# Kernel optimization log

Hardware: AMD Instinct MI355X
Metric: run time of the kernel (lower is better)

The kernel has to match this reference:

```python
import jax, jax.numpy as jnp
import numpy as np

D_MODEL = 256
D_STATE = 128          # d_model // 2
D_CONV = 4
EXPAND = 4
D_INNER = EXPAND * D_MODEL  # 1024
DT_RANK = (D_MODEL + 15) // 16  # 16
N_HEADS = 8
D_FF = 4 * D_MODEL
EPS = 1e-6


def layer_norm(x, a, b):
    # torch LayerNorm-like but with unbiased std (ddof=1) per the source
    mean = jnp.mean(x, axis=-1, keepdims=True)
    d = x.shape[-1]
    var = jnp.sum((x - mean) ** 2, axis=-1, keepdims=True) / (d - 1)
    std = jnp.sqrt(var)
    return a * (x - mean) / (std + EPS) + b


def silu(x):
    return x * jax.nn.sigmoid(x)


def mamba(x, in_proj_w, conv_w, conv_b, x_proj_w, dt_proj_w, dt_proj_b, A_log, Dp, out_proj_w):
    B, L, _ = x.shape
    xz = jnp.einsum('bld,ed->ble', x, in_proj_w)  # (B,L,2*D_INNER)
    xi, z = xz[..., :D_INNER], xz[..., D_INNER:]
    # causal depthwise conv1d over L
    xp = jnp.pad(xi, ((0, 0), (D_CONV - 1, 0), (0, 0)))
    u = conv_b
    for k in range(D_CONV):
        u = u + xp[:, k:k + L, :] * conv_w[:, k]
    u = silu(u)  # (B,L,D_INNER)
    dbl = jnp.einsum('bld,ed->ble', u, x_proj_w)  # (B,L,DT_RANK+2*D_STATE)
    dt = dbl[..., :DT_RANK]
    Bm = dbl[..., DT_RANK:DT_RANK + D_STATE]
    Cm = dbl[..., DT_RANK + D_STATE:]
    dt = jax.nn.softplus(jnp.einsum('blr,dr->bld', dt, dt_proj_w) + dt_proj_b)  # (B,L,D_INNER)
    A = -jnp.exp(A_log)  # (D_INNER, D_STATE)
    dA = jnp.exp(jnp.einsum('bld,dn->bldn', dt, A))          # (B,L,Din,N)
    dBu = jnp.einsum('bld,bln,bld->bldn', dt, Bm, u)          # (B,L,Din,N)

    def step(h, inp):
        dA_t, dBu_t, C_t = inp
        h = dA_t * h + dBu_t                    # (B,Din,N)
        y = jnp.einsum('bdn,bn->bd', h, C_t)    # (B,Din)
        return h, y

    h0 = jnp.zeros((B, D_INNER, D_STATE), dtype=x.dtype)
    _, ys = jax.lax.scan(step, h0, (jnp.swapaxes(dA, 0, 1), jnp.swapaxes(dBu, 0, 1), jnp.swapaxes(Cm, 0, 1)))
    y = jnp.swapaxes(ys, 0, 1) + u * Dp  # (B,L,Din)
    y = y * silu(z)
    return jnp.einsum('ble,de->bld', y, out_proj_w)


def cross_attention(q_in, kv_in, mask, wq_w, wq_b, wk_w, wk_b, wv_w, wv_b, wo_w, wo_b):
    B, Lq, _ = q_in.shape
    Lk = kv_in.shape[1]
    dk = D_MODEL // N_HEADS
    q = (jnp.einsum('bld,ed->ble', q_in, wq_w) + wq_b).reshape(B, Lq, N_HEADS, dk).transpose(0, 2, 1, 3)
    k = (jnp.einsum('bld,ed->ble', kv_in, wk_w) + wk_b).reshape(B, Lk, N_HEADS, dk).transpose(0, 2, 1, 3)
    v = (jnp.einsum('bld,ed->ble', kv_in, wv_w) + wv_b).reshape(B, Lk, N_HEADS, dk).transpose(0, 2, 1, 3)
    scores = jnp.einsum('bhqd,bhkd->bhqk', q, k) / np.sqrt(dk)
    # mask: (B,1,Lk) bool -> broadcast (B,1,1,Lk)
    scores = jnp.where(mask[:, None, :, :], scores, jnp.finfo(scores.dtype).min)
    p = jax.nn.softmax(scores, axis=-1)
    o = jnp.einsum('bhqk,bhkd->bhqd', p, v).transpose(0, 2, 1, 3).reshape(B, Lq, D_MODEL)
    return jnp.einsum('ble,de->bld', o, wo_w) + wo_b


def setup_inputs() -> dict:
    key = jax.random.key(0)
    ks = jax.random.split(key, 24)
    s = 0.02
    B, L, Lm = 2, 512, 512
    inp = {
        'x': jax.random.normal(ks[0], (B, L, D_MODEL), jnp.float32),
        'memory': jax.random.normal(ks[1], (B, Lm, D_MODEL), jnp.float32),
        'src_mask': jnp.ones((B, 1, Lm), bool),
        'tgt_mask': jnp.ones((B, 1, L), bool),
        # mamba params
        'in_proj_w': jax.random.normal(ks[2], (2 * D_INNER, D_MODEL)) * s,
        'conv_w': jax.random.normal(ks[3], (D_INNER, D_CONV)) * s,
        'conv_b': jnp.zeros((D_INNER,)),
        'x_proj_w': jax.random.normal(ks[4], (DT_RANK + 2 * D_STATE, D_INNER)) * s,
        'dt_proj_w': jax.random.normal(ks[5], (D_INNER, DT_RANK)) * s,
        'dt_proj_b': jnp.log(jnp.expm1(0.01)) * jnp.ones((D_INNER,)),
        'A_log': jnp.log(jnp.broadcast_to(jnp.arange(1, D_STATE + 1, dtype=jnp.float32), (D_INNER, D_STATE))),
        'Dp': jnp.ones((D_INNER,)),
        'out_proj_w': jax.random.normal(ks[6], (D_MODEL, D_INNER)) * s,
        # norms
        'norm1_a': jnp.ones((D_MODEL,)), 'norm1_b': jnp.zeros((D_MODEL,)),
        'norm2_a': jnp.ones((D_MODEL,)), 'norm2_b': jnp.zeros((D_MODEL,)),
        'norm3_a': jnp.ones((D_MODEL,)), 'norm3_b': jnp.zeros((D_MODEL,)),
        # cross attention
        'wq_w': jax.random.normal(ks[7], (D_MODEL, D_MODEL)) * s, 'wq_b': jnp.zeros((D_MODEL,)),
        'wk_w': jax.random.normal(ks[8], (D_MODEL, D_MODEL)) * s, 'wk_b': jnp.zeros((D_MODEL,)),
        'wv_w': jax.random.normal(ks[9], (D_MODEL, D_MODEL)) * s, 'wv_b': jnp.zeros((D_MODEL,)),
        'wo_w': jax.random.normal(ks[10], (D_MODEL, D_MODEL)) * s, 'wo_b': jnp.zeros((D_MODEL,)),
        # ffn
        'w1_w': jax.random.normal(ks[11], (D_FF, D_MODEL)) * s, 'w1_b': jnp.zeros((D_FF,)),
        'w2_w': jax.random.normal(ks[12], (D_MODEL, D_FF)) * s, 'w2_b': jnp.zeros((D_MODEL,)),
    }
    return inp


def reference(x, memory, src_mask, tgt_mask,
              in_proj_w, conv_w, conv_b, x_proj_w, dt_proj_w, dt_proj_b, A_log, Dp, out_proj_w,
              norm1_a, norm1_b, norm2_a, norm2_b, norm3_a, norm3_b,
              wq_w, wq_b, wk_w, wk_b, wv_w, wv_b, wo_w, wo_b,
              w1_w, w1_b, w2_w, w2_b):
    # self mamba block (pre-norm, residual); dropout = 0
    h = x + mamba(layer_norm(x, norm1_a, norm1_b), in_proj_w, conv_w, conv_b,
                  x_proj_w, dt_proj_w, dt_proj_b, A_log, Dp, out_proj_w)
    # cross attention block
    h = h + cross_attention(layer_norm(h, norm2_a, norm2_b), memory, src_mask,
                            wq_w, wq_b, wk_w, wk_b, wv_w, wv_b, wo_w, wo_b)
    # ffn block
    hn = layer_norm(h, norm3_a, norm3_b)
    ff = jnp.einsum('blf,df->bld', jax.nn.relu(jnp.einsum('bld,fd->blf', hn, w1_w) + w1_b), w2_w) + w2_b
    return h + ff
```

## Files before the change

### kernel.cpp

```cpp
#include <hip/hip_runtime.h>
#include <hip/hip_bf16.h>

#define B_SZ 2
#define L_SEQ 512
#define D_MODEL 256
#define D_STATE 128
#define D_CONV 4
#define D_INNER 1024
#define DT_RANK 16
#define N_HEADS 8
#define DK 32
#define D_FF 1024
#define R_TOT (B_SZ * L_SEQ)
#define DBL_LD (DT_RANK + 2 * D_STATE)
#define NSEG 16
#define SEGL 32

typedef __hip_bfloat16 bf16;
typedef __attribute__((ext_vector_type(8))) short short8;
typedef __attribute__((ext_vector_type(4))) float floatx4;

__device__ inline float fexp(float x) { return __expf(x); }
__device__ inline float frcp(float x) { return __builtin_amdgcn_rcpf(x); }
__device__ inline float silu_f(float x) { return x * frcp(1.f + fexp(-x)); }
__device__ inline float softplus_f(float x) { return (x > 20.f) ? x : __logf(1.f + fexp(x)); }
__device__ inline float bf2f(unsigned short u) { return __uint_as_float(((unsigned)u) << 16); }

__device__ inline float dpp_sum64(float x) {
    x += __int_as_float(__builtin_amdgcn_update_dpp(0, __float_as_int(x), 0x111, 0xf, 0xf, true));
    x += __int_as_float(__builtin_amdgcn_update_dpp(0, __float_as_int(x), 0x112, 0xf, 0xf, true));
    x += __int_as_float(__builtin_amdgcn_update_dpp(0, __float_as_int(x), 0x114, 0xf, 0xf, true));
    x += __int_as_float(__builtin_amdgcn_update_dpp(0, __float_as_int(x), 0x118, 0xf, 0xf, true));
    x += __int_as_float(__builtin_amdgcn_update_dpp(0, __float_as_int(x), 0x142, 0xf, 0xf, true));
    x += __int_as_float(__builtin_amdgcn_update_dpp(0, __float_as_int(x), 0x143, 0xf, 0xf, true));
    return x;
}

#define S_MEM 262144
#define S_INW 524288
#define S_XPW 278528
#define S_OPW 262144
#define S_WQ  65536
#define S_WK  65536
#define S_WV  65536
#define S_WO  65536
#define S_W1  262144
#define S_W2  262144
#define S_TOT (S_MEM+S_INW+S_XPW+S_OPW+S_WQ+S_WK+S_WV+S_WO+S_W1+S_W2)
#define PACK_BLKS ((S_TOT + 255) / 256)
#define Z1_F4 (4 * R_TOT * D_MODEL / 4)
#define Z2_F4 (R_TOT * D_MODEL / 4)
#define Z3_F4 (R_TOT * DBL_LD / 4)
#define ZERO_BLKS ((Z1_F4 + Z2_F4 + Z3_F4 + 255) / 256)

__global__ __launch_bounds__(256) void pack_ln1(
    const float* __restrict__ s0, const float* __restrict__ s1,
    const float* __restrict__ s2, const float* __restrict__ s3,
    const float* __restrict__ s4, const float* __restrict__ s5,
    const float* __restrict__ s6, const float* __restrict__ s7,
    const float* __restrict__ s8, const float* __restrict__ s9,
    bf16* __restrict__ dst,
    const float* __restrict__ X, const float* __restrict__ a,
    const float* __restrict__ bvec, bf16* __restrict__ ln1b,
    float* __restrict__ zero1, float* __restrict__ zero2,
    float* __restrict__ zero3)
{
    __shared__ float r1[256], r2[256];
    if (blockIdx.x < PACK_BLKS) {
        const long i = (long)blockIdx.x * 256 + threadIdx.x;
        if (i >= S_TOT) return;
        const long off[11] = {0, S_MEM, S_MEM+S_INW, S_MEM+S_INW+S_XPW,
            S_MEM+S_INW+S_XPW+S_OPW, S_MEM+S_INW+S_XPW+S_OPW+S_WQ,
            S_MEM+S_INW+S_XPW+S_OPW+S_WQ+S_WK,
            S_MEM+S_INW+S_XPW+S_OPW+S_WQ+S_WK+S_WV,
            S_MEM+S_INW+S_XPW+S_OPW+S_WQ+S_WK+S_WV+S_WO,
            S_MEM+S_INW+S_XPW+S_OPW+S_WQ+S_WK+S_WV+S_WO+S_W1, S_TOT};
        const float* srcs[10] = {s0,s1,s2,s3,s4,s5,s6,s7,s8,s9};
        int seg = 0;
#pragma unroll
        for (int k = 1; k < 10; ++k) if (i >= off[k]) seg = k;
        dst[i] = __float2bfloat16(srcs[seg][i - off[seg]]);
    } else if (blockIdx.x < PACK_BLKS + R_TOT) {
        const int row = blockIdx.x - PACK_BLKS;
        const int t = threadIdx.x;
        const float v = X[(long)row * D_MODEL + t];
        r1[t] = v;
        r2[t] = v * v;
        __syncthreads();
        for (int s = 128; s > 0; s >>= 1) {
            if (t < s) { r1[t] += r1[t + s]; r2[t] += r2[t + s]; }
            __syncthreads();
        }
        const float mean = r1[0] * (1.f / 256.f);
        const float var = (r2[0] - 256.f * mean * mean) * (1.f / 255.f);
        const float sd = sqrtf(fmaxf(var, 0.f));
        const float o = a[t] * (v - mean) / (sd + 1e-6f) + bvec[t];
        ln1b[(long)row * D_MODEL + t] = __float2bfloat16(o);
    } else {
        const long i4 = (long)(blockIdx.x - PACK_BLKS - R_TOT) * 256 + threadIdx.x;
        const float4 z = {0.f, 0.f, 0.f, 0.f};
        if (i4 < Z1_F4)                      *(float4*)&zero1[i4 * 4] = z;
        else if (i4 < Z1_F4 + Z2_F4)          *(float4*)&zero2[(i4 - Z1_F4) * 4] = z;
        else if (i4 < Z1_F4 + Z2_F4 + Z3_F4)  *(float4*)&zero3[(i4 - Z1_F4 - Z2_F4) * 4] = z;
    }
}

template <int EPI>
__global__ __launch_bounds__(256) void mfma_gemm(
    const bf16* __restrict__ A, const bf16* __restrict__ W, int K,
    float* __restrict__ C, bf16* __restrict__ Cb, int ldc,
    const float* __restrict__ bias, const float* __restrict__ res,
    int M, int N)
{
    const int wave = threadIdx.x >> 6;
    const int lane = threadIdx.x & 63;
    const int row16 = lane & 15;
    const int quad  = lane >> 4;
    const int bm = blockIdx.y * 64 + wave * 16;
    const int bn = blockIdx.x * 64;

    floatx4 acc[4];
#pragma unroll
    for (int t = 0; t < 4; ++t) acc[t] = (floatx4){0.f, 0.f, 0.f, 0.f};

    const long arow = (long)(bm + row16) * K;
    for (int k0 = 0; k0 < K; k0 += 32) {
        const short8 av = *(const short8*)(A + arow + k0 + quad * 8);
#pragma unroll
        for (int t = 0; t < 4; ++t) {
            const int gn = bn + t * 16 + row16;
            short8 bv = {0,0,0,0,0,0,0,0};
            if (gn < N) bv = *(const short8*)(W + (long)gn * K + k0 + quad * 8);
            acc[t] = __builtin_amdgcn_mfma_f32_16x16x32_bf16(av, bv, acc[t], 0, 0, 0);
        }
    }

#pragma unroll
    for (int t = 0; t < 4; ++t) {
        const int gn = bn + t * 16 + row16;
        if (gn >= N) continue;
        const float bs = bias ? bias[gn] : 0.f;
#pragma unroll
        for (int r = 0; r < 4; ++r) {
            const int gm = bm + quad * 4 + r;
            float v = acc[t][r] + bs;
            if (EPI == 1) v = fmaxf(v, 0.f);
            const long ci = (long)gm * ldc + gn;
            if (res) v += res[ci];
            if (C)  C[ci] = v;
            if (Cb) Cb[ci] = __float2bfloat16(v);
        }
    }
}

template <int SK>
__global__ __launch_bounds__(256) void splitk_gemm(
    const bf16* __restrict__ A, const bf16* __restrict__ W, int K,
    float* __restrict__ C, int ldc,
    const float* __restrict__ bias, const float* __restrict__ res,
    int M, int N)
{
    const int wave = threadIdx.x >> 6;
    const int lane = threadIdx.x & 63;
    const int row16 = lane & 15;
    const int quad  = lane >> 4;
    const int bm = blockIdx.y * 64 + wave * 16;
    const int bn = blockIdx.x * 64;
    const int kz = blockIdx.z;
    const int ksl = K / SK;
    const int kbeg = kz * ksl;

    floatx4 acc[4];
#pragma unroll
    for (int t = 0; t < 4; ++t) acc[t] = (floatx4){0.f, 0.f, 0.f, 0.f};

    const long arow = (long)(bm + row16) * K;
    for (int k0 = kbeg; k0 < kbeg + ksl; k0 += 32) {
        const short8 av = *(const short8*)(A + arow + k0 + quad * 8);
#pragma unroll
        for (int t = 0; t < 4; ++t) {
            const int gn = bn + t * 16 + row16;
            short8 bv = {0,0,0,0,0,0,0,0};
            if (gn < N) bv = *(const short8*)(W + (long)gn * K + k0 + quad * 8);
            acc[t] = __builtin_amdgcn_mfma_f32_16x16x32_bf16(av, bv, acc[t], 0, 0, 0);
        }
    }

#pragma unroll
    for (int t = 0; t < 4; ++t) {
        const int gn = bn + t * 16 + row16;
        if (gn >= N) continue;
        const float bs = (kz == 0 && bias) ? bias[gn] : 0.f;
#pragma unroll
        for (int r = 0; r < 4; ++r) {
            const int gm = bm + quad * 4 + r;
            float v = acc[t][r] + bs;
            const long ci = (long)gm * ldc + gn;
            if (kz == 0 && res) v += res[ci];
            atomicAdd(&C[ci], v);
        }
    }
}

__global__ __launch_bounds__(256) void xproj_kv_gemm(
    const bf16* __restrict__ ub, const bf16* __restrict__ XPWb,
    float* __restrict__ dbl,
    const bf16* __restrict__ memb, const bf16* __restrict__ WKb,
    const bf16* __restrict__ WVb,
    const float* __restrict__ WKB, const float* __restrict__ WVB,
    float* __restrict__ kb, float* __restrict__ vb)
{
    const int wave = threadIdx.x >> 6;
    const int lane = threadIdx.x & 63;
    const int row16 = lane & 15;
    const int quad  = lane >> 4;
    const int bm = blockIdx.y * 64 + wave * 16;
    const int bn = blockIdx.x * 64;
    const int z = blockIdx.z;

    const bf16* A; const bf16* W; const float* bias; float* C;
    int K, N, ldc, kbeg, ksl;
    if (z < 4) {
        A = ub; W = XPWb; bias = nullptr; C = dbl;
        K = D_INNER; N = DBL_LD; ldc = DBL_LD;
        ksl = D_INNER / 4; kbeg = z * ksl;
    } else {
        if (bn >= D_MODEL) return;
        const int zz = z - 4;
        const int which = zz >> 1;
        const int kz = zz & 1;
        A = memb; W = which ? WVb : WKb;
        bias = (kz == 0) ? (which ? WVB : WKB) : nullptr;
        C = which ? vb : kb;
        K = D_MODEL; N = D_MODEL; ldc = D_MODEL;
        ksl = D_MODEL / 2; kbeg = kz * ksl;
    }

    floatx4 acc[4];
#pragma unroll
    for (int t = 0; t < 4; ++t) acc[t] = (floatx4){0.f, 0.f, 0.f, 0.f};

    const long arow = (long)(bm + row16) * K;
    for (int k0 = kbeg; k0 < kbeg + ksl; k0 += 32) {
        const short8 av = *(const short8*)(A + arow + k0 + quad * 8);
#pragma unroll
        for (int t = 0; t < 4; ++t) {
            const int gn = bn + t * 16 + row16;
            short8 bv = {0,0,0,0,0,0,0,0};
            if (gn < N) bv = *(const short8*)(W + (long)gn * K + k0 + quad * 8);
            acc[t] = __builtin_amdgcn_mfma_f32_16x16x32_bf16(av, bv, acc[t], 0, 0, 0);
        }
    }

#pragma unroll
    for (int t = 0; t < 4; ++t) {
        const int gn = bn + t * 16 + row16;
        if (gn >= N) continue;
        const float bs = bias ? bias[gn] : 0.f;
#pragma unroll
        for (int r = 0; r < 4; ++r) {
            const int gm = bm + quad * 4 + r;
            atomicAdd(&C[(long)gm * ldc + gn], acc[t][r] + bs);
        }
    }
}

__global__ __launch_bounds__(256) void q_gemm(
    const bf16* __restrict__ ln2b, const bf16* __restrict__ WQb,
    const float* __restrict__ WQB, float* __restrict__ qb)
{
    const int wave = threadIdx.x >> 6;
    const int lane = threadIdx.x & 63;
    const int row16 = lane & 15;
    const int quad  = lane >> 4;
    const int bm = blockIdx.y * 64 + wave * 16;
    const int bn = blockIdx.x * 64;
    const int kz = blockIdx.z;
    const int kbeg = kz * (D_MODEL / 2);

    floatx4 acc[4];
#pragma unroll
    for (int t = 0; t < 4; ++t) acc[t] = (floatx4){0.f, 0.f, 0.f, 0.f};

    const long arow = (long)(bm + row16) * D_MODEL;
    for (int k0 = kbeg; k0 < kbeg + D_MODEL / 2; k0 += 32) {
        const short8 av = *(const short8*)(ln2b + arow + k0 + quad * 8);
#pragma unroll
        for (int t = 0; t < 4; ++t) {
            const int gn = bn + t * 16 + row16;
            const short8 bv = *(const short8*)(WQb + (long)gn * D_MODEL + k0 + quad * 8);
            acc[t] = __builtin_amdgcn_mfma_f32_16x16x32_bf16(av, bv, acc[t], 0, 0, 0);
        }
    }
#pragma unroll
    for (int t = 0; t < 4; ++t) {
        const int gn = bn + t * 16 + row16;
        const float bs = (kz == 0) ? WQB[gn] : 0.f;
#pragma unroll
        for (int r = 0; r < 4; ++r) {
            const int gm = bm + quad * 4 + r;
            atomicAdd(&qb[(long)gm * D_MODEL + gn], acc[t][r] + bs);
        }
    }
}

__global__ __launch_bounds__(256) void gemm16_ln(
    const bf16* __restrict__ A, const bf16* __restrict__ W, int K,
    const float* __restrict__ bias, const float* __restrict__ res,
    float* __restrict__ Cf,
    const float* __restrict__ lna, const float* __restrict__ lnb,
    bf16* __restrict__ lnout)
{
    __shared__ float tile[16][264];
    __shared__ float red1[16][16];
    __shared__ float red2[16][16];
    const int w = threadIdx.x >> 6;
    const int lane = threadIdx.x & 63;
    const int row16 = lane & 15;
    const int quad  = lane >> 4;
    const int bm = blockIdx.x * 16;

    floatx4 acc[4];
#pragma unroll
    for (int t = 0; t < 4; ++t) acc[t] = (floatx4){0.f, 0.f, 0.f, 0.f};

    const long arow = (long)(bm + row16) * K;
    for (int k0 = 0; k0 < K; k0 += 32) {
        const short8 av = *(const short8*)(A + arow + k0 + quad * 8);
#pragma unroll
        for (int t = 0; t < 4; ++t) {
            const int gn = w * 64 + t * 16 + row16;
            const short8 bv = *(const short8*)(W + (long)gn * K + k0 + quad * 8);
            acc[t] = __builtin_amdgcn_mfma_f32_16x16x32_bf16(av, bv, acc[t], 0, 0, 0);
        }
    }

#pragma unroll
    for (int t = 0; t < 4; ++t) {
        const int gn = w * 64 + t * 16 + row16;
        const float bs = bias ? bias[gn] : 0.f;
#pragma unroll
        for (int r = 0; r < 4; ++r) {
            const int gm = bm + quad * 4 + r;
            float v = acc[t][r] + bs;
            const long ci = (long)gm * D_MODEL + gn;
            if (res) v += res[ci];
            Cf[ci] = v;
            tile[quad * 4 + r][gn] = v;
        }
    }
    __syncthreads();

    const int r = threadIdx.x >> 4;
    const int g = threadIdx.x & 15;
    float s = 0.f, q = 0.f;
#pragma unroll
    for (int i = 0; i < 16; ++i) {
        const float x = tile[r][g * 16 + i];
        s += x; q += x * x;
    }
    red1[r][g] = s; red2[r][g] = q;
    __syncthreads();
    float ts = 0.f, tq = 0.f;
#pragma unroll
    for (int i = 0; i < 16; ++i) { ts += red1[r][i]; tq += red2[r][i]; }
    const float mean = ts * (1.f / 256.f);
    const float var = (tq - 256.f * mean * mean) * (1.f / 255.f);
    const float sd = sqrtf(fmaxf(var, 0.f));
    const long rowbase = (long)(bm + r) * D_MODEL;
#pragma unroll
    for (int i = 0; i < 16; ++i) {
        const int c = g * 16 + i;
        const float o = lna[c] * (tile[r][c] - mean) / (sd + 1e-6f) + lnb[c];
        lnout[rowbase + c] = __float2bfloat16(o);
    }
}

__global__ __launch_bounds__(256) void ln_kernel(
    const float* __restrict__ x, const float* __restrict__ a,
    const float* __restrict__ bvec, bf16* __restrict__ out)
{
    const int row = blockIdx.x;
    const int t = threadIdx.x;
    const float v = x[(long)row * D_MODEL + t];
    __shared__ float r1[256], r2[256];
    r1[t] = v;
    r2[t] = v * v;
    __syncthreads();
    for (int s = 128; s > 0; s >>= 1) {
        if (t < s) { r1[t] += r1[t + s]; r2[t] += r2[t + s]; }
        __syncthreads();
    }
    const float mean = r1[0] * (1.f / 256.f);
    const float var = (r2[0] - 256.f * mean * mean) * (1.f / 255.f);
    const float sd = sqrtf(fmaxf(var, 0.f));
    const float o = a[t] * (v - mean) / (sd + 1e-6f) + bvec[t];
    out[(long)row * D_MODEL + t] = __float2bfloat16(o);
}

__global__ __launch_bounds__(256) void dt_gemm_T(
    const float* __restrict__ A , const float* __restrict__ W ,
    const float* __restrict__ bias, float* __restrict__ dtT)
{
    __shared__ float As[DT_RANK][65];
    __shared__ float Bs[DT_RANK][65];
    __shared__ float Ct[64][65];
    const int bm = blockIdx.y * 64;
    const int bn = blockIdx.x * 64;
    const int tid = threadIdx.x;
    const int tx = tid & 15;
    const int ty = tid >> 4;
    const int r = tid >> 2;
    const int kk = (tid & 3) * 4;
#pragma unroll
    for (int q = 0; q < 4; ++q) {
        As[kk + q][r] = A[(long)(bm + r) * DBL_LD + kk + q];
        Bs[kk + q][r] = W[(long)(bn + r) * DT_RANK + kk + q];
    }
    __syncthreads();
    float acc[4][4] = {};
#pragma unroll
    for (int k = 0; k < DT_RANK; ++k) {
        float a[4], bv[4];
#pragma unroll
        for (int i = 0; i < 4; ++i) a[i] = As[k][ty * 4 + i];
#pragma unroll
        for (int j = 0; j < 4; ++j) bv[j] = Bs[k][tx * 4 + j];
#pragma unroll
        for (int i = 0; i < 4; ++i)
#pragma unroll
            for (int j = 0; j < 4; ++j)
                acc[i][j] = fmaf(a[i], bv[j], acc[i][j]);
    }
#pragma unroll
    for (int i = 0; i < 4; ++i)
#pragma unroll
        for (int j = 0; j < 4; ++j)
            Ct[tx * 4 + j][ty * 4 + i] = softplus_f(acc[i][j] + bias[bn + tx * 4 + j]);
    __syncthreads();
    const int b = bm >> 9;
    const int l0 = bm & 511;
    const int r2 = tid >> 4;
    const int c4 = (tid & 15) * 4;
#pragma unroll
    for (int q = 0; q < 4; ++q) {
        const int dl = r2 + q * 16;
        float4 v = {Ct[dl][c4], Ct[dl][c4 + 1], Ct[dl][c4 + 2], Ct[dl][c4 + 3]};
        *(float4*)&dtT[((long)(b * D_INNER + bn + dl) << 9) + l0 + c4] = v;
    }
}

__global__ __launch_bounds__(256) void conv_silu_T(
    const bf16* __restrict__ xz, const float* __restrict__ cw,
    const float* __restrict__ cb, bf16* __restrict__ ub, float* __restrict__ uT)
{
    __shared__ float t[64][65];
    const int db = blockIdx.x;
    const int lb = blockIdx.y;
    const int b  = blockIdx.z;
    const int tid = threadIdx.x;
    const int r  = tid >> 4;
    const int c4 = (tid & 15) * 4;
    const int d0 = db * 64 + c4;

    const float4 cb4 = *(const float4*)&cb[d0];
    float cwa[4][4];
#pragma unroll
    for (int i = 0; i < 4; ++i) {
        const float4 w = *(const float4*)&cw[(d0 + i) * 4];
        cwa[i][0] = w.x; cwa[i][1] = w.y; cwa[i][2] = w.z; cwa[i][3] = w.w;
    }

#pragma unroll
    for (int q = 0; q < 4; ++q) {
        const int ll = r + q * 16;
        const int l = lb * 64 + ll;
        float s0 = cb4.x, s1 = cb4.y, s2 = cb4.z, s3 = cb4.w;
#pragma unroll
        for (int k = 0; k < D_CONV; ++k) {
            const int ls = l - 3 + k;
            if (ls >= 0) {
                const ushort4 xv = *(const ushort4*)&xz[((long)(b * L_SEQ + ls)) * (2 * D_INNER) + d0];
                s0 = fmaf(bf2f(xv.x), cwa[0][k], s0);
                s1 = fmaf(bf2f(xv.y), cwa[1][k], s1);
                s2 = fmaf(bf2f(xv.z), cwa[2][k], s2);
                s3 = fmaf(bf2f(xv.w), cwa[3][k], s3);
            }
        }
        s0 = silu_f(s0); s1 = silu_f(s1); s2 = silu_f(s2); s3 = silu_f(s3);
        bf16 b0 = __float2bfloat16(s0), b1 = __float2bfloat16(s1);
        bf16 b2 = __float2bfloat16(s2), b3 = __float2bfloat16(s3);
        ushort4 pk;
        pk.x = *reinterpret_cast<unsigned short*>(&b0);
        pk.y = *reinterpret_cast<unsigned short*>(&b1);
        pk.z = *reinterpret_cast<unsigned short*>(&b2);
        pk.w = *reinterpret_cast<unsigned short*>(&b3);
        *reinterpret_cast<ushort4*>(ub + ((long)(b * L_SEQ + l)) * D_INNER + d0) = pk;
        t[c4 + 0][ll] = s0; t[c4 + 1][ll] = s1;
        t[c4 + 2][ll] = s2; t[c4 + 3][ll] = s3;
    }
    __syncthreads();
#pragma unroll
    for (int q = 0; q < 4; ++q) {
        const int dl = r + q * 16;
        float4 v = {t[dl][c4], t[dl][c4 + 1], t[dl][c4 + 2], t[dl][c4 + 3]};
        *(float4*)&uT[((long)(b * D_INNER + db * 64 + dl) << 9) + lb * 64 + c4] = v;
    }
}

__global__ __launch_bounds__(1024) void scan_fused(
    const float* __restrict__ dtT, const float* __restrict__ uT,
    const float* __restrict__ dbl, const float* __restrict__ A_log,
    float* __restrict__ ysT)
{
    const int cd = blockIdx.x;
    const int b = cd >> 10;
    const int d = cd & 1023;
    const int w = threadIdx.x >> 6;
    const int lane = threadIdx.x & 63;
    const int n0 = lane * 2;

    __shared__ float Sh[NSEG][D_STATE];
    __shared__ float Ph[NSEG][D_STATE];

    const float An0 = -fexp(A_log[(long)d * D_STATE + n0]);
    const float An1 = -fexp(A_log[(long)d * D_STATE + n0 + 1]);

    const float* dtp = dtT + ((long)cd << 9) + w * SEGL;
    const float* up  = uT  + ((long)cd << 9) + w * SEGL;
    const float* blp = dbl + ((long)(b * L_SEQ + w * SEGL)) * DBL_LD + DT_RANK + n0;
    const float* clp = blp + D_STATE;

    if (w < NSEG - 1) {
        float h0 = 0.f, h1 = 0.f, sdt = 0.f;
        for (int s = 0; s < SEGL / 8; ++s) {
            const float4 dt0 = *(const float4*)(dtp + s * 8);
            const float4 dt1 = *(const float4*)(dtp + s * 8 + 4);
            const float4 u0  = *(const float4*)(up + s * 8);
            const float4 u1  = *(const float4*)(up + s * 8 + 4);
            float2 Bv[8];
#pragma unroll
            for (int j = 0; j < 8; ++j)
                Bv[j] = *(const float2*)(blp + (long)(s * 8 + j) * DBL_LD);
            const float dts[8] = {dt0.x, dt0.y, dt0.z, dt0.w, dt1.x, dt1.y, dt1.z, dt1.w};
            const float us[8]  = {u0.x,  u0.y,  u0.z,  u0.w,  u1.x,  u1.y,  u1.z,  u1.w};
#pragma unroll
            for (int j = 0; j < 8; ++j) {
                const float dtv = dts[j];
                sdt += dtv;
                const float dtu = dtv * us[j];
                h0 = fmaf(fexp(dtv * An0), h0, dtu * Bv[j].x);
                h1 = fmaf(fexp(dtv * An1), h1, dtu * Bv[j].y);
            }
        }
        Sh[w][n0] = h0; Sh[w][n0 + 1] = h1;
        Ph[w][n0] = fexp(An0 * sdt); Ph[w][n0 + 1] = fexp(An1 * sdt);
    }
    __syncthreads();

    float h0 = 0.f, h1 = 0.f;
    for (int s = 0; s < w; ++s) {
        h0 = fmaf(Ph[s][n0],     h0, Sh[s][n0]);
        h1 = fmaf(Ph[s][n0 + 1], h1, Sh[s][n0 + 1]);
    }

    float* ysp = ysT + ((long)cd << 9) + w * SEGL;
    for (int s = 0; s < SEGL / 8; ++s) {
        const float4 dt0 = *(const float4*)(dtp + s * 8);
        const float4 dt1 = *(const float4*)(dtp + s * 8 + 4);
        const float4 u0  = *(const float4*)(up + s * 8);
        const float4 u1  = *(const float4*)(up + s * 8 + 4);
        float2 Bv[8], Cv[8];
#pragma unroll
        for (int j = 0; j < 8; ++j) {
            Bv[j] = *(const float2*)(blp + (long)(s * 8 + j) * DBL_LD);
            Cv[j] = *(const float2*)(clp + (long)(s * 8 + j) * DBL_LD);
        }
        const float dts[8] = {dt0.x, dt0.y, dt0.z, dt0.w, dt1.x, dt1.y, dt1.z, dt1.w};
        const float us[8]  = {u0.x,  u0.y,  u0.z,  u0.w,  u1.x,  u1.y,  u1.z,  u1.w};
        float yp[8];
#pragma unroll
        for (int j = 0; j < 8; ++j) {
            const float dtv = dts[j];
            const float dtu = dtv * us[j];
            h0 = fmaf(fexp(dtv * An0), h0, dtu * Bv[j].x);
            h1 = fmaf(fexp(dtv * An1), h1, dtu * Bv[j].y);
            yp[j] = fmaf(h0, Cv[j].x, h1 * Cv[j].y);
        }
#pragma unroll
        for (int j = 0; j < 8; ++j) yp[j] = dpp_sum64(yp[j]);

        if (lane == 63) {
            *(float4*)(ysp + s * 8)     = (float4){yp[0], yp[1], yp[2], yp[3]};
            *(float4*)(ysp + s * 8 + 4) = (float4){yp[4], yp[5], yp[6], yp[7]};
        }
    }
}

__global__ __launch_bounds__(256) void gate_kernel(
    const float* __restrict__ ysT, const float* __restrict__ uT,
    const float* __restrict__ Dp, const bf16* __restrict__ xz,
    bf16* __restrict__ y)
{
    __shared__ float t[64][65];
    __shared__ float t2[64][65];
    const int db = blockIdx.x;
    const int lb = blockIdx.y;
    const int b  = blockIdx.z;
    const int tid = threadIdx.x;
    const int r  = tid >> 4;
    const int c4 = (tid & 15) * 4;

#pragma unroll
    for (int q = 0; q < 4; ++q) {
        const int dr = r + q * 16;
        const long base = (((long)(b * D_INNER + db * 64 + dr)) << 9) + lb * 64 + c4;
        const float4 v = *(const float4*)&ysT[base];
        const float4 w = *(const float4*)&uT[base];
        t[dr][c4 + 0] = v.x; t[dr][c4 + 1] = v.y;
        t[dr][c4 + 2] = v.z; t[dr][c4 + 3] = v.w;
        t2[dr][c4 + 0] = w.x; t2[dr][c4 + 1] = w.y;
        t2[dr][c4 + 2] = w.z; t2[dr][c4 + 3] = w.w;
    }
    __syncthreads();

    const float4 dp4 = *(const float4*)&Dp[db * 64 + c4];
#pragma unroll
    for (int q = 0; q < 4; ++q) {
        const int lr = r + q * 16;
        const long row = (long)b * L_SEQ + lb * 64 + lr;
        const ushort4 zu = *(const ushort4*)&xz[row * 2 * D_INNER + D_INNER + db * 64 + c4];
        const float r0 = (t[c4 + 0][lr] + t2[c4 + 0][lr] * dp4.x) * silu_f(bf2f(zu.x));
        const float r1 = (t[c4 + 1][lr] + t2[c4 + 1][lr] * dp4.y) * silu_f(bf2f(zu.y));
        const float r2 = (t[c4 + 2][lr] + t2[c4 + 2][lr] * dp4.z) * silu_f(bf2f(zu.z));
        const float r3 = (t[c4 + 3][lr] + t2[c4 + 3][lr] * dp4.w) * silu_f(bf2f(zu.w));
        bf16 b0 = __float2bfloat16(r0), b1 = __float2bfloat16(r1);
        bf16 b2 = __float2bfloat16(r2), b3 = __float2bfloat16(r3);
        ushort4 pk;
        pk.x = *reinterpret_cast<unsigned short*>(&b0);
        pk.y = *reinterpret_cast<unsigned short*>(&b1);
        pk.z = *reinterpret_cast<unsigned short*>(&b2);
        pk.w = *reinterpret_cast<unsigned short*>(&b3);
        *reinterpret_cast<ushort4*>(y + row * D_INNER + db * 64 + c4) = pk;
    }
}

#define QT 16
#define CK 64

__global__ __launch_bounds__(256) void attn_kernel(
    const float* __restrict__ q, const float* __restrict__ k,
    const float* __restrict__ v, bf16* __restrict__ o)
{
    const int qt = blockIdx.x;
    const int hh = blockIdx.y;
    const int b  = blockIdx.z;
    const int t = threadIdx.x;
    const int lane = t & 15;
    const int qa = t >> 4;
    const int q0 = qt * QT + qa;

    __shared__ float Ks[CK][36];
    __shared__ float Vs[CK][36];

    const float scale = 0.17677669529663687f;
    float qr0[32];
    {
        const float* q0p = q + ((long)(b * L_SEQ + q0) * D_MODEL + hh * DK);
#pragma unroll
        for (int i = 0; i < 8; ++i) {
            const float4 a = *(const float4*)&q0p[i * 4];
            qr0[i*4+0] = a.x * scale; qr0[i*4+1] = a.y * scale;
            qr0[i*4+2] = a.z * scale; qr0[i*4+3] = a.w * scale;
        }
    }

    float m0 = -1e30f, l0 = 0.f, o0[32] = {};

    for (int c = 0; c < L_SEQ; c += CK) {
        __syncthreads();
        {
            const int fid = t * 2;
            const int row = fid >> 3;
            const int c0  = (fid & 7) * 4;
            const float* kp = k + ((long)(b * L_SEQ + c + row) * D_MODEL + hh * DK + c0);
            const float* vp = v + ((long)(b * L_SEQ + c + row) * D_MODEL + hh * DK + c0);
            *(float4*)&Ks[row][c0]     = *(const float4*)kp;
            *(float4*)&Ks[row][c0 + 4] = *(const float4*)(kp + 4);
            *(float4*)&Vs[row][c0]     = *(const float4*)vp;
            *(float4*)&Vs[row][c0 + 4] = *(const float4*)(vp + 4);
        }
        __syncthreads();

        float s0[4];
#pragma unroll
        for (int i = 0; i < 4; ++i) {
            const int kk = i * 16 + lane;
            float a0 = 0.f;
#pragma unroll
            for (int dd = 0; dd < 32; dd += 4) {
                const float4 kv = *(const float4*)&Ks[kk][dd];
                a0 = fmaf(qr0[dd+0], kv.x, a0); a0 = fmaf(qr0[dd+1], kv.y, a0);
                a0 = fmaf(qr0[dd+2], kv.z, a0); a0 = fmaf(qr0[dd+3], kv.w, a0);
            }
            s0[i] = a0;
        }

        float cm0 = s0[0];
#pragma unroll
        for (int i = 1; i < 4; ++i) cm0 = fmaxf(cm0, s0[i]);
#pragma unroll
        for (int off = 8; off > 0; off >>= 1)
            cm0 = fmaxf(cm0, __shfl_down(cm0, off, 16));
        cm0 = __shfl(cm0, 0, 16);

        const float nm0 = fmaxf(m0, cm0);
        const float al0 = fexp(m0 - nm0);
        l0 *= al0;
#pragma unroll
        for (int dd = 0; dd < 32; ++dd) o0[dd] *= al0;
        m0 = nm0;

        float p0[4];
#pragma unroll
        for (int i = 0; i < 4; ++i) { p0[i] = fexp(s0[i] - m0); l0 += p0[i]; }

#pragma unroll
        for (int i = 0; i < 4; ++i) {
            const int kk = i * 16 + lane;
#pragma unroll
            for (int dd = 0; dd < 32; dd += 4) {
                const float4 vv = *(const float4*)&Vs[kk][dd];
                o0[dd+0] = fmaf(p0[i], vv.x, o0[dd+0]);
                o0[dd+1] = fmaf(p0[i], vv.y, o0[dd+1]);
                o0[dd+2] = fmaf(p0[i], vv.z, o0[dd+2]);
                o0[dd+3] = fmaf(p0[i], vv.w, o0[dd+3]);
            }
        }
    }

#pragma unroll
    for (int off = 8; off > 0; off >>= 1) {
        l0 += __shfl_down(l0, off, 16);
#pragma unroll
        for (int dd = 0; dd < 32; ++dd) o0[dd] += __shfl_down(o0[dd], off, 16);
    }
    if (lane == 0) {
        const float i0 = 1.f / l0;
        bf16* op0 = o + ((long)(b * L_SEQ + q0) * D_MODEL + hh * DK);
#pragma unroll
        for (int dd = 0; dd < 32; ++dd) op0[dd] = __float2bfloat16(o0[dd] * i0);
    }
}


extern "C" void kernel_launch(void* const* d_in, const int* in_sizes, int n_in,
                              void* d_out, int out_size, void* d_ws, size_t ws_size,
                              hipStream_t stream) {
    const float* X   = (const float*)d_in[0];
    const float* MEM = (const float*)d_in[1];
    const float* CW  = (const float*)d_in[5];
    const float* CB  = (const float*)d_in[6];
    const float* DTW = (const float*)d_in[8];
    const float* DTB = (const float*)d_in[9];
    const float* ALG = (const float*)d_in[10];
    const float* DP  = (const float*)d_in[11];
    const float* N1A = (const float*)d_in[13];
    const float* N1B = (const float*)d_in[14];
    const float* N2A = (const float*)d_in[15];
    const float* N2B = (const float*)d_in[16];
    const float* N3A = (const float*)d_in[17];
    const float* N3B = (const float*)d_in[18];
    const float* WQB = (const float*)d_in[20];
    const float* WKB = (const float*)d_in[22];
    const float* WVB = (const float*)d_in[24];
    const float* WOB = (const float*)d_in[26];
    const float* W1B = (const float*)d_in[28];
    const float* W2B = (const float*)d_in[30];
    const float* INW = (const float*)d_in[4];
    const float* XPW = (const float*)d_in[7];
    const float* OPW = (const float*)d_in[12];
    const float* WQ  = (const float*)d_in[19];
    const float* WKw = (const float*)d_in[21];
    const float* WVw = (const float*)d_in[23];
    const float* WO  = (const float*)d_in[25];
    const float* W1  = (const float*)d_in[27];
    const float* W2  = (const float*)d_in[29];
    float* out = (float*)d_out;

    bf16* bp = (bf16*)d_ws;
    bf16* ub   = bp;  bp += (long)R_TOT * D_INNER;
    bf16* ybb  = bp;  bp += (long)R_TOT * D_INNER;
    bf16* ffab = ybb;
    bf16* xzb  = bp;  bp += (long)R_TOT * 2 * D_INNER;
    bf16* ln1b = bp;  bp += (long)R_TOT * D_MODEL;
    bf16* aob  = ln1b;
    bf16* ln2b = bp;  bp += (long)R_TOT * D_MODEL;
    bf16* ln3b = ln2b;
    bf16* arena = bp; bp += S_TOT;
    bf16* MEMb = arena;
    bf16* INWb = MEMb + S_MEM;
    bf16* XPWb = INWb + S_INW;
    bf16* OPWb = XPWb + S_XPW;
    bf16* WQb  = OPWb + S_OPW;
    bf16* WKb  = WQb + S_WQ;
    bf16* WVb  = WKb + S_WK;
    bf16* WOb  = WVb + S_WV;
    bf16* W1b  = WOb + S_WO;
    bf16* W2b  = W1b + S_W1;

    float* p = (float*)(bp + ((((long)(bp - (bf16*)d_ws)) & 1) ? 1 : 0));
    float* uT  = p;                                  p += (long)R_TOT * D_INNER;
    float* dbl = p;                                  p += (long)R_TOT * DBL_LD;
    float* dtT = p;                                  p += (long)R_TOT * D_INNER;
    float* ysT = p;                                  p += (long)R_TOT * D_INNER;
    float* h1  = p;                                  p += (long)R_TOT * D_MODEL;
    float* qb  = p;                                  p += (long)R_TOT * D_MODEL;
    float* kb  = p;                                  p += (long)R_TOT * D_MODEL;
    float* vb  = p;                                  p += (long)R_TOT * D_MODEL;
    float* h2  = p;                                  p += (long)R_TOT * D_MODEL;

    const dim3 blk256(256);
    const int MT64 = R_TOT / 64;

    pack_ln1<<<PACK_BLKS + R_TOT + ZERO_BLKS, blk256, 0, stream>>>(
        MEM, INW, XPW, OPW, WQ, WKw, WVw, WO, W1, W2, arena,
        X, N1A, N1B, ln1b, h1, out, dbl);

    mfma_gemm<0><<<dim3(2 * D_INNER / 64, MT64), blk256, 0, stream>>>(
        ln1b, INWb, D_MODEL, nullptr, xzb, 2 * D_INNER, nullptr, nullptr,
        R_TOT, 2 * D_INNER);

    conv_silu_T<<<dim3(D_INNER / 64, L_SEQ / 64, B_SZ), blk256, 0, stream>>>(
        xzb, CW, CB, ub, uT);

    xproj_kv_gemm<<<dim3((DBL_LD + 63) / 64, MT64, 8), blk256, 0, stream>>>(
        ub, XPWb, dbl, MEMb, WKb, WVb, WKB, WVB, kb, vb);

    dt_gemm_T<<<dim3(D_INNER / 64, MT64), blk256, 0, stream>>>(dbl, DTW, DTB, dtT);

    scan_fused<<<B_SZ * D_INNER, dim3(1024), 0, stream>>>(dtT, uT, dbl, ALG, ysT);

    gate_kernel<<<dim3(D_INNER / 64, L_SEQ / 64, B_SZ), blk256, 0, stream>>>(
        ysT, uT, DP, xzb, ybb);

    splitk_gemm<4><<<dim3(D_MODEL / 64, MT64, 4), blk256, 0, stream>>>(
        ybb, OPWb, D_INNER, h1, D_MODEL, nullptr, X, R_TOT, D_MODEL);

    ln_kernel<<<R_TOT, blk256, 0, stream>>>(h1, N2A, N2B, ln2b);

    q_gemm<<<dim3(D_MODEL / 64, MT64, 2), blk256, 0, stream>>>(ln2b, WQb, WQB, qb);

    attn_kernel<<<dim3(L_SEQ / QT, N_HEADS, B_SZ), blk256, 0, stream>>>(qb, kb, vb, aob);

    gemm16_ln<<<R_TOT / 16, blk256, 0, stream>>>(
        aob, WOb, D_MODEL, WOB, h1, h2, N3A, N3B, ln3b);

    mfma_gemm<1><<<dim3(D_FF / 64, MT64), blk256, 0, stream>>>(
        ln3b, W1b, D_MODEL, nullptr, ffab, D_FF, W1B, nullptr, R_TOT, D_FF);

    splitk_gemm<4><<<dim3(D_MODEL / 64, MT64, 4), blk256, 0, stream>>>(
        ffab, W2b, D_FF, out, D_MODEL, W2B, h2, R_TOT, D_MODEL);

    (void)in_sizes; (void)n_in; (void)out_size; (void)ws_size;
}
```

Baseline: 376.2 us.

## Process four channels per scan block and use transpose-reduce for outputs

The selective scan kernel now handles four D_INNER channels per block, so each B/C row load from dbl is reused across four channels and fewer blocks are launched. The per-timestep 64-lane reduction is replaced by a butterfly transpose-reduce (bpermute, ds_swizzle, dpp) that reduces eight outputs at once. Exponentials switch to exp2 with A pre-scaled by log2(e). The cost is more registers per thread and lower occupancy at 1024 threads per block, plus scattered scalar stores for ys.

```diff
diff --git a/kernel.cpp b/kernel.cpp
--- a/kernel.cpp
+++ b/kernel.cpp
@@ -15,12 +15,14 @@
 #define DBL_LD (DT_RANK + 2 * D_STATE)
 #define NSEG 16
 #define SEGL 32
+#define DPB 4
 
 typedef __hip_bfloat16 bf16;
 typedef __attribute__((ext_vector_type(8))) short short8;
 typedef __attribute__((ext_vector_type(4))) float floatx4;
 
 __device__ inline float fexp(float x) { return __expf(x); }
+__device__ inline float fexp2(float x) { return __builtin_amdgcn_exp2f(x); }
 __device__ inline float frcp(float x) { return __builtin_amdgcn_rcpf(x); }
 __device__ inline float silu_f(float x) { return x * frcp(1.f + fexp(-x)); }
 __device__ inline float softplus_f(float x) { return (x > 20.f) ? x : __logf(1.f + fexp(x)); }
@@ -34,6 +36,13 @@
     x += __int_as_float(__builtin_amdgcn_update_dpp(0, __float_as_int(x), 0x142, 0xf, 0xf, true));
     x += __int_as_float(__builtin_amdgcn_update_dpp(0, __float_as_int(x), 0x143, 0xf, 0xf, true));
     return x;
+}
+
+__device__ inline float swz_xor16(float x) {
+    return __int_as_float(__builtin_amdgcn_ds_swizzle(__float_as_int(x), 0x401F));
+}
+__device__ inline float swz_xor8(float x) {
+    return __int_as_float(__builtin_amdgcn_ds_swizzle(__float_as_int(x), 0x201F));
 }
 
 #define S_MEM 262144
@@ -513,86 +522,130 @@
     const float* __restrict__ dbl, const float* __restrict__ A_log,
     float* __restrict__ ysT)
 {
-    const int cd = blockIdx.x;
-    const int b = cd >> 10;
-    const int d = cd & 1023;
+    const int b  = blockIdx.x >> 8;
+    const int d0 = (blockIdx.x & 255) * DPB;
     const int w = threadIdx.x >> 6;
     const int lane = threadIdx.x & 63;
     const int n0 = lane * 2;
 
-    __shared__ float Sh[NSEG][D_STATE];
-    __shared__ float Ph[NSEG][D_STATE];
-
-    const float An0 = -fexp(A_log[(long)d * D_STATE + n0]);
-    const float An1 = -fexp(A_log[(long)d * D_STATE + n0 + 1]);
-
-    const float* dtp = dtT + ((long)cd << 9) + w * SEGL;
-    const float* up  = uT  + ((long)cd << 9) + w * SEGL;
+    __shared__ float Sh[NSEG][DPB][D_STATE];
+    __shared__ float Ph[NSEG][DPB][D_STATE];
+
+    float An0[DPB], An1[DPB];
+#pragma unroll
+    for (int di = 0; di < DPB; ++di) {
+        An0[di] = -fexp(A_log[(long)(d0 + di) * D_STATE + n0]) * 1.44269504f;
+        An1[di] = -fexp(A_log[(long)(d0 + di) * D_STATE + n0 + 1]) * 1.44269504f;
+    }
+
     const float* blp = dbl + ((long)(b * L_SEQ + w * SEGL)) * DBL_LD + DT_RANK + n0;
     const float* clp = blp + D_STATE;
+    const long tbase = ((long)(b * D_INNER + d0) << 9) + w * SEGL;
 
     if (w < NSEG - 1) {
-        float h0 = 0.f, h1 = 0.f, sdt = 0.f;
+        float h0[DPB] = {}, h1[DPB] = {}, sdt[DPB] = {};
         for (int s = 0; s < SEGL / 8; ++s) {
-            const float4 dt0 = *(const float4*)(dtp + s * 8);
-            const float4 dt1 = *(const float4*)(dtp + s * 8 + 4);
-            const float4 u0  = *(const float4*)(up + s * 8);
-            const float4 u1  = *(const float4*)(up + s * 8 + 4);
             float2 Bv[8];
 #pragma unroll
             for (int j = 0; j < 8; ++j)
                 Bv[j] = *(const float2*)(blp + (long)(s * 8 + j) * DBL_LD);
-            const float dts[8] = {dt0.x, dt0.y, dt0.z, dt0.w, dt1.x, dt1.y, dt1.z, dt1.w};
-            const float us[8]  = {u0.x,  u0.y,  u0.z,  u0.w,  u1.x,  u1.y,  u1.z,  u1.w};
-#pragma unroll
-            for (int j = 0; j < 8; ++j) {
-                const float dtv = dts[j];
-                sdt += dtv;
-                const float dtu = dtv * us[j];
-                h0 = fmaf(fexp(dtv * An0), h0, dtu * Bv[j].x);
-                h1 = fmaf(fexp(dtv * An1), h1, dtu * Bv[j].y);
+#pragma unroll
+            for (int di = 0; di < DPB; ++di) {
+                const float* dtp = dtT + tbase + ((long)di << 9) + s * 8;
+                const float* up  = uT  + tbase + ((long)di << 9) + s * 8;
+                const float4 dt0 = *(const float4*)dtp;
+                const float4 dt1 = *(const float4*)(dtp + 4);
+                const float4 u0  = *(const float4*)up;
+                const float4 u1  = *(const float4*)(up + 4);
+                const float dts[8] = {dt0.x, dt0.y, dt0.z, dt0.w, dt1.x, dt1.y, dt1.z, dt1.w};
+                const float us[8]  = {u0.x,  u0.y,  u0.z,  u0.w,  u1.x,  u1.y,  u1.z,  u1.w};
+#pragma unroll
+                for (int j = 0; j < 8; ++j) {
+                    const float dtv = dts[j];
+                    sdt[di] += dtv;
+                    const float dtu = dtv * us[j];
+                    h0[di] = fmaf(fexp2(dtv * An0[di]), h0[di], dtu * Bv[j].x);
+                    h1[di] = fmaf(fexp2(dtv * An1[di]), h1[di], dtu * Bv[j].y);
+                }
             }
         }
-        Sh[w][n0] = h0; Sh[w][n0 + 1] = h1;
-        Ph[w][n0] = fexp(An0 * sdt); Ph[w][n0 + 1] = fexp(An1 * sdt);
+#pragma unroll
+        for (int di = 0; di < DPB; ++di) {
+            Sh[w][di][n0]     = h0[di];
+            Sh[w][di][n0 + 1] = h1[di];
+            Ph[w][di][n0]     = fexp2(An0[di] * sdt[di]);
+            Ph[w][di][n0 + 1] = fexp2(An1[di] * sdt[di]);
+        }
     }
     __syncthreads();
 
-    float h0 = 0.f, h1 = 0.f;
+    float h0[DPB] = {}, h1[DPB] = {};
     for (int s = 0; s < w; ++s) {
-        h0 = fmaf(Ph[s][n0],     h0, Sh[s][n0]);
-        h1 = fmaf(Ph[s][n0 + 1], h1, Sh[s][n0 + 1]);
-    }
-
-    float* ysp = ysT + ((long)cd << 9) + w * SEGL;
+#pragma unroll
+        for (int di = 0; di < DPB; ++di) {
+            h0[di] = fmaf(Ph[s][di][n0],     h0[di], Sh[s][di][n0]);
+            h1[di] = fmaf(Ph[s][di][n0 + 1], h1[di], Sh[s][di][n0 + 1]);
+        }
+    }
+
+    const int bpa = (lane ^ 32) << 2;
+    const bool lo32 = lane < 32;
+    const bool b16 = (lane & 16) != 0;
+    const bool b8  = (lane & 8) != 0;
+    const int g = lane >> 3;
+    const bool wl = (lane & 7) == 7;
+
     for (int s = 0; s < SEGL / 8; ++s) {
-        const float4 dt0 = *(const float4*)(dtp + s * 8);
-        const float4 dt1 = *(const float4*)(dtp + s * 8 + 4);
-        const float4 u0  = *(const float4*)(up + s * 8);
-        const float4 u1  = *(const float4*)(up + s * 8 + 4);
         float2 Bv[8], Cv[8];
 #pragma unroll
         for (int j = 0; j < 8; ++j) {
             Bv[j] = *(const float2*)(blp + (long)(s * 8 + j) * DBL_LD);
             Cv[j] = *(const float2*)(clp + (long)(s * 8 + j) * DBL_LD);
         }
-        const float dts[8] = {dt0.x, dt0.y, dt0.z, dt0.w, dt1.x, dt1.y, dt1.z, dt1.w};
-        const float us[8]  = {u0.x,  u0.y,  u0.z,  u0.w,  u1.x,  u1.y,  u1.z,  u1.w};
-        float yp[8];
-#pragma unroll
-        for (int j = 0; j < 8; ++j) {
-            const float dtv = dts[j];
-            const float dtu = dtv * us[j];
-            h0 = fmaf(fexp(dtv * An0), h0, dtu * Bv[j].x);
-            h1 = fmaf(fexp(dtv * An1), h1, dtu * Bv[j].y);
-            yp[j] = fmaf(h0, Cv[j].x, h1 * Cv[j].y);
-        }
-#pragma unroll
-        for (int j = 0; j < 8; ++j) yp[j] = dpp_sum64(yp[j]);
-
-        if (lane == 63) {
-            *(float4*)(ysp + s * 8)     = (float4){yp[0], yp[1], yp[2], yp[3]};
-            *(float4*)(ysp + s * 8 + 4) = (float4){yp[4], yp[5], yp[6], yp[7]};
+#pragma unroll
+        for (int di = 0; di < DPB; ++di) {
+            const float* dtp = dtT + tbase + ((long)di << 9) + s * 8;
+            const float* up  = uT  + tbase + ((long)di << 9) + s * 8;
+            const float4 dt0 = *(const float4*)dtp;
+            const float4 dt1 = *(const float4*)(dtp + 4);
+            const float4 u0  = *(const float4*)up;
+            const float4 u1  = *(const float4*)(up + 4);
+            const float dts[8] = {dt0.x, dt0.y, dt0.z, dt0.w, dt1.x, dt1.y, dt1.z, dt1.w};
+            const float us[8]  = {u0.x,  u0.y,  u0.z,  u0.w,  u1.x,  u1.y,  u1.z,  u1.w};
+            float yp[8];
+#pragma unroll
+            for (int j = 0; j < 8; ++j) {
+                const float dtv = dts[j];
+                const float dtu = dtv * us[j];
+                h0[di] = fmaf(fexp2(dtv * An0[di]), h0[di], dtu * Bv[j].x);
+                h1[di] = fmaf(fexp2(dtv * An1[di]), h1[di], dtu * Bv[j].y);
+                yp[j] = fmaf(h0[di], Cv[j].x, h1[di] * Cv[j].y);
+            }
+            float z0[4];
+#pragma unroll
+            for (int j = 0; j < 4; ++j) {
+                const float t = lo32 ? yp[j]     : yp[j + 4];
+                const float u = lo32 ? yp[j + 4] : yp[j];
+                z0[j] = t + __int_as_float(
+                    __builtin_amdgcn_ds_bpermute(bpa, __float_as_int(u)));
+            }
+            float z1[2];
+#pragma unroll
+            for (int j = 0; j < 2; ++j) {
+                const float t = b16 ? z0[j + 2] : z0[j];
+                const float u = b16 ? z0[j]     : z0[j + 2];
+                z1[j] = t + swz_xor16(u);
+            }
+            float z2;
+            {
+                const float t = b8 ? z1[1] : z1[0];
+                const float u = b8 ? z1[0] : z1[1];
+                z2 = t + swz_xor8(u);
+            }
+            z2 += __int_as_float(__builtin_amdgcn_update_dpp(0, __float_as_int(z2), 0x111, 0xf, 0xf, true));
+            z2 += __int_as_float(__builtin_amdgcn_update_dpp(0, __float_as_int(z2), 0x112, 0xf, 0xf, true));
+            z2 += __int_as_float(__builtin_amdgcn_update_dpp(0, __float_as_int(z2), 0x114, 0xf, 0xf, true));
+            if (wl) ysT[tbase + ((long)di << 9) + s * 8 + g] = z2;
         }
     }
 }
@@ -839,7 +892,7 @@
 
     dt_gemm_T<<<dim3(D_INNER / 64, MT64), blk256, 0, stream>>>(dbl, DTW, DTB, dtT);
 
-    scan_fused<<<B_SZ * D_INNER, dim3(1024), 0, stream>>>(dtT, uT, dbl, ALG, ysT);
+    scan_fused<<<B_SZ * D_INNER / DPB, dim3(1024), 0, stream>>>(dtT, uT, dbl, ALG, ysT);
 
     gate_kernel<<<dim3(D_INNER / 64, L_SEQ / 64, B_SZ), blk256, 0, stream>>>(
         ysT, uT, DP, xzb, ybb);
```

Result: faster. 321.8 us (-14.5%).
